# Performance work log

Hardware: AMD Instinct MI355X
Metric: run time of the kernel (lower is better)

## Reference

```python
import jax, jax.numpy as jnp
import numpy as np

B, S, D, H = 8, 2048, 1024, 64


def setup_inputs() -> dict:
    key = jax.random.key(0)
    ks = jax.random.split(key, 9)
    s = 0.02
    return {
        "x": jax.random.normal(ks[0], (B, S, D), jnp.float32),
        "Wq": jax.random.normal(ks[1], (H, D), jnp.float32) * s,
        "bq": jnp.zeros((H,), jnp.float32),
        "Wk": jax.random.normal(ks[2], (H, D), jnp.float32) * s,
        "bk": jnp.zeros((H,), jnp.float32),
        "Wv": jax.random.normal(ks[3], (H, D), jnp.float32) * s,
        "bv": jnp.zeros((H,), jnp.float32),
        "Wo": jax.random.normal(ks[4], (H, H), jnp.float32) * s,
        "bo": jnp.zeros((H,), jnp.float32),
    }


def reference(x, Wq, bq, Wk, bk, Wv, bv, Wo, bo):
    # Linear layers: y = x @ W.T + b (torch nn.Linear convention)
    q = jnp.einsum("bsd,hd->bsh", x, Wq) + bq  # [B,S,H]
    k = jnp.einsum("bsd,hd->bsh", x, Wk) + bk
    v = jnp.einsum("bsd,hd->bsh", x, Wv) + bv
    scale = jnp.float32(H) ** 0.5
    scores = jnp.einsum("bsh,bth->bst", q, k) / scale  # [B,S,S]
    causal = jnp.tril(jnp.ones((S, S), bool))
    scores = jnp.where(causal, scores, -jnp.inf)
    attn = jax.nn.softmax(scores, axis=-1)
    out = jnp.einsum("bst,bth->bsh", attn, v)  # [B,S,H]
    out = jnp.einsum("bsh,gh->bsg", out, Wo) + bo  # output proj [H,H]
    return out
```

## Files before the change

kernel.cpp:

```cpp
#include <hip/hip_runtime.h>
#include <hip/hip_bf16.h>

#define NB 8
#define NS 2048
#define ND 1024
#define NH 64
#define NM (NB*NS)

typedef __attribute__((ext_vector_type(8))) short short8;
typedef __attribute__((ext_vector_type(4))) short short4v;
typedef __attribute__((ext_vector_type(4))) float f32x4;
typedef __attribute__((ext_vector_type(4))) float f4;

#define QSCALE (0.125f * 1.44269504088896340736f)

__device__ __forceinline__ unsigned short f2bf(float f) {
    union { __hip_bfloat16 h; unsigned short u; } cv;
    cv.h = __float2bfloat16(f);
    return cv.u;
}

__global__ __launch_bounds__(256) void convw_kernel(
    const float* __restrict__ Wq, const float* __restrict__ bq,
    const float* __restrict__ Wk, const float* __restrict__ bk,
    const float* __restrict__ Wv, const float* __restrict__ bv,
    const float* __restrict__ Wo,
    unsigned short* __restrict__ Wb, unsigned short* __restrict__ Wob,
    float* __restrict__ biasb)
{
    const int row = blockIdx.x;
    const int t = threadIdx.x;
    if (row < 192) {
        const float* W = row < 64 ? Wq : (row < 128 ? Wk : Wv);
        const float sc = row < 64 ? QSCALE : 1.0f;
        f4 v = *(const f4*)&W[(size_t)(row & 63) * ND + t * 4];
        short4v o;
#pragma unroll
        for (int j = 0; j < 4; ++j) o[j] = (short)f2bf(v[j] * sc);
        *(short4v*)&Wb[(size_t)row * ND + t * 4] = o;
        if (row == 0 && t < 192) {
            const float* bsrc = t < 64 ? bq : (t < 128 ? bk : bv);
            biasb[t] = bsrc[t & 63] * (t < 64 ? QSCALE : 1.0f);
        }
    } else if (t < 16) {
        f4 v = *(const f4*)&Wo[(size_t)(row - 192) * 64 + t * 4];
        short4v o;
#pragma unroll
        for (int j = 0; j < 4; ++j) o[j] = (short)f2bf(v[j]);
        *(short4v*)&Wob[(size_t)(row - 192) * 64 + t * 4] = o;
    }
}

__global__ __launch_bounds__(512, 2) void qkv_kernel(
    const float* __restrict__ x, const unsigned short* __restrict__ Wb,
    const float* __restrict__ biasb,
    unsigned short* __restrict__ q, unsigned short* __restrict__ k,
    unsigned short* __restrict__ vT)
{
    __shared__ unsigned short As[2][64 * 64];
    __shared__ unsigned short Bs[2][192 * 64];

    const int t = threadIdx.x;
    const int lane = t & 63, g = lane >> 4, li = lane & 15;
    const int w = t >> 6, rg = w >> 2, cg = w & 3;
    const int m0 = blockIdx.x * 64;
    const int arow = t >> 3, ach = t & 7;

    f32x4 acc[2][3];
#pragma unroll
    for (int a = 0; a < 2; ++a)
#pragma unroll
        for (int nf = 0; nf < 3; ++nf) acc[a][nf] = (f32x4)0.f;

    f4 xa[2][2]; short8 wr[2][3];

#define QKV_LOAD(KS, SL)                                                          \
    {                                                                             \
        const float* p_ = &x[(size_t)(m0 + arow) * ND + (KS) * 64 + ach * 8];     \
        xa[SL][0] = *(const f4*)p_; xa[SL][1] = *(const f4*)(p_ + 4);             \
        wr[SL][0] = *(const short8*)&Wb[(size_t)(t >> 3) * ND + (KS) * 64 + (t & 7) * 8];                  \
        wr[SL][1] = *(const short8*)&Wb[(size_t)((t + 512) >> 3) * ND + (KS) * 64 + ((t + 512) & 7) * 8];  \
        wr[SL][2] = *(const short8*)&Wb[(size_t)((t + 1024) >> 3) * ND + (KS) * 64 + ((t + 1024) & 7) * 8];\
    }

#define QKV_COMMIT(SL, BUF)                                                       \
    {                                                                             \
        short8 av_;                                                               \
        for (int j_ = 0; j_ < 4; ++j_) {                                          \
            av_[j_] = (short)f2bf(xa[SL][0][j_]);                                 \
            av_[j_ + 4] = (short)f2bf(xa[SL][1][j_]);                             \
        }                                                                         \
        *(short8*)&As[BUF][arow * 64 + ((ach ^ (arow & 7)) << 3)] = av_;          \
        int r0_ = t >> 3, c0_ = t & 7;                                            \
        *(short8*)&Bs[BUF][r0_ * 64 + ((c0_ ^ (r0_ & 7)) << 3)] = wr[SL][0];      \
        int r1_ = (t + 512) >> 3, c1_ = (t + 512) & 7;                            \
        *(short8*)&Bs[BUF][r1_ * 64 + ((c1_ ^ (r1_ & 7)) << 3)] = wr[SL][1];      \
        int r2_ = (t + 1024) >> 3, c2_ = (t + 1024) & 7;                          \
        *(short8*)&Bs[BUF][r2_ * 64 + ((c2_ ^ (r2_ & 7)) << 3)] = wr[SL][2];      \
    }

    QKV_LOAD(0, 0);
    QKV_LOAD(1, 1);
    QKV_COMMIT(0, 0);
    __syncthreads();

#pragma unroll
    for (int ks = 0; ks < 16; ++ks) {
        const int cur = ks & 1;
        if (ks < 14) QKV_LOAD(ks + 2, cur);
#pragma unroll
        for (int h = 0; h < 2; ++h) {
            short8 af0 = *(const short8*)&As[cur][(rg * 32 + 0 + li) * 64 + (((g + 4 * h) ^ (li & 7)) << 3)];
            short8 af1 = *(const short8*)&As[cur][(rg * 32 + 16 + li) * 64 + (((g + 4 * h) ^ (li & 7)) << 3)];
#pragma unroll
            for (int nf = 0; nf < 3; ++nf) {
                short8 bf = *(const short8*)&Bs[cur][(cg * 48 + nf * 16 + li) * 64 + (((g + 4 * h) ^ (li & 7)) << 3)];
                acc[0][nf] = __builtin_amdgcn_mfma_f32_16x16x32_bf16(af0, bf, acc[0][nf], 0, 0, 0);
                acc[1][nf] = __builtin_amdgcn_mfma_f32_16x16x32_bf16(af1, bf, acc[1][nf], 0, 0, 0);
            }
        }
        if (ks < 15) QKV_COMMIT((ks + 1) & 1, cur ^ 1);
        __syncthreads();
    }

#pragma unroll
    for (int nf = 0; nf < 3; ++nf) {
        const int col = cg * 48 + nf * 16 + li;
        const float bias = biasb[col];
#pragma unroll
        for (int a = 0; a < 2; ++a) {
            const int row0 = m0 + rg * 32 + a * 16 + 4 * g;
            if (col < 64) {
#pragma unroll
                for (int i = 0; i < 4; ++i)
                    q[(size_t)(row0 + i) * NH + col] = f2bf(acc[a][nf][i] + bias);
            } else if (col < 128) {
#pragma unroll
                for (int i = 0; i < 4; ++i)
                    k[(size_t)(row0 + i) * NH + (col - 64)] = f2bf(acc[a][nf][i] + bias);
            } else {
                short4v pk;
#pragma unroll
                for (int i = 0; i < 4; ++i) pk[i] = (short)f2bf(acc[a][nf][i] + bias);
                const int bb = row0 >> 11, s = row0 & 2047;
                *(short4v*)&vT[(size_t)(bb * NH + (col - 128)) * NS + s] = pk;
            }
        }
    }
}

__global__ __launch_bounds__(256, 2) void attn_kernel(
    const unsigned short* __restrict__ q, const unsigned short* __restrict__ k,
    const unsigned short* __restrict__ vT,
    float* __restrict__ Opart, float* __restrict__ lpart,
    int ctLog, int MAXC)
{
    __shared__ unsigned short Ks[2][64 * 64];
    __shared__ unsigned short Vs[2][64 * 64];
    __shared__ unsigned short Ps[4][16 * 64];

    const int t = threadIdx.x;
    const int w = t >> 6, lane = t & 63, g = lane >> 4, li = lane & 15;
    const int b = blockIdx.x & 7;
    const int pid = blockIdx.x >> 3;
    const int CT = 1 << ctLog;

    int qt = 0, c = 0;
    {
        int acc = 0;
        for (int u = 31; u >= 0; --u) {
            int nch = (u + CT) >> ctLog;
            if (pid < acc + nch) { qt = u; c = pid - acc; break; }
            acc += nch;
        }
    }
    const int t0 = c * CT;
    const int rem = qt + 1 - t0;
    const int tcount = rem < CT ? rem : CT;

    const size_t qkbase = (size_t)b * NS * NH;
    const int qrow = qt * 64 + w * 16 + li;
    const short8 qa0 = *(const short8*)&q[qkbase + (size_t)qrow * NH + g * 8];
    const short8 qa1 = *(const short8*)&q[qkbase + (size_t)qrow * NH + 32 + g * 8];

    float l_i[4]; f32x4 oacc[4];
#pragma unroll
    for (int i = 0; i < 4; ++i) { l_i[i] = 0.f; oacc[i] = (f32x4)0.f; }

    const int srow = t >> 3, sch = t & 7;
    short8 kreg0, kreg1, vreg0, vreg1;

    {
        const int kv0 = t0 * 64;
        kreg0 = *(const short8*)&k[qkbase + (size_t)(kv0 + srow) * NH + sch * 8];
        kreg1 = *(const short8*)&k[qkbase + (size_t)(kv0 + srow + 32) * NH + sch * 8];
        vreg0 = *(const short8*)&vT[(size_t)(b * NH + srow) * NS + kv0 + sch * 8];
        vreg1 = *(const short8*)&vT[(size_t)(b * NH + srow + 32) * NS + kv0 + sch * 8];
        *(short8*)&Ks[0][srow * 64 + ((sch ^ (srow & 7)) << 3)] = kreg0;
        *(short8*)&Ks[0][(srow + 32) * 64 + ((sch ^ (srow & 7)) << 3)] = kreg1;
        *(short8*)&Vs[0][srow * 64 + ((sch ^ (srow & 7)) << 3)] = vreg0;
        *(short8*)&Vs[0][(srow + 32) * 64 + ((sch ^ (srow & 7)) << 3)] = vreg1;
    }
    __syncthreads();

    for (int tt = 0; tt < tcount; ++tt) {
        const int cur = tt & 1;
        const int kv0 = (t0 + tt) * 64;
        if (tt + 1 < tcount) {
            const int nv0 = kv0 + 64;
            kreg0 = *(const short8*)&k[qkbase + (size_t)(nv0 + srow) * NH + sch * 8];
            kreg1 = *(const short8*)&k[qkbase + (size_t)(nv0 + srow + 32) * NH + sch * 8];
            vreg0 = *(const short8*)&vT[(size_t)(b * NH + srow) * NS + nv0 + sch * 8];
            vreg1 = *(const short8*)&vT[(size_t)(b * NH + srow + 32) * NS + nv0 + sch * 8];
        }
        f32x4 s[4];
#pragma unroll
        for (int c4 = 0; c4 < 4; ++c4) {
            s[c4] = (f32x4)0.f;
            const int krow = 16 * c4 + li;
            short8 kf0 = *(const short8*)&Ks[cur][krow * 64 + ((g ^ (li & 7)) << 3)];
            s[c4] = __builtin_amdgcn_mfma_f32_16x16x32_bf16(qa0, kf0, s[c4], 0, 0, 0);
            short8 kf1 = *(const short8*)&Ks[cur][krow * 64 + (((g + 4) ^ (li & 7)) << 3)];
            s[c4] = __builtin_amdgcn_mfma_f32_16x16x32_bf16(qa1, kf1, s[c4], 0, 0, 0);
        }
        if (kv0 == qt * 64) {
#pragma unroll
            for (int c4 = 0; c4 < 4; ++c4)
#pragma unroll
                for (int i = 0; i < 4; ++i)
                    if (16 * c4 + li > w * 16 + 4 * g + i) s[c4][i] = -1e30f;
        }
        float p[4][4];
#pragma unroll
        for (int c4 = 0; c4 < 4; ++c4)
#pragma unroll
            for (int i = 0; i < 4; ++i)
                p[c4][i] = exp2f(fminf(s[c4][i], 80.f));
#pragma unroll
        for (int i = 0; i < 4; ++i)
            l_i[i] += (p[0][i] + p[1][i]) + (p[2][i] + p[3][i]);

#pragma unroll
        for (int c4 = 0; c4 < 4; ++c4)
#pragma unroll
            for (int i = 0; i < 4; ++i) {
                const int prow = 4 * g + i;
                const int chunk = 2 * c4 + (li >> 3);
                Ps[w][prow * 64 + ((chunk ^ (prow & 7)) << 3) + (li & 7)] = f2bf(p[c4][i]);
            }
        short8 pf0 = *(const short8*)&Ps[w][li * 64 + ((g ^ (li & 7)) << 3)];
        short8 pf1 = *(const short8*)&Ps[w][li * 64 + (((g + 4) ^ (li & 7)) << 3)];
#pragma unroll
        for (int nf = 0; nf < 4; ++nf) {
            const int vrow = nf * 16 + li;
            short8 vf0 = *(const short8*)&Vs[cur][vrow * 64 + ((g ^ (li & 7)) << 3)];
            short8 vf1 = *(const short8*)&Vs[cur][vrow * 64 + (((g + 4) ^ (li & 7)) << 3)];
            oacc[nf] = __builtin_amdgcn_mfma_f32_16x16x32_bf16(pf0, vf0, oacc[nf], 0, 0, 0);
            oacc[nf] = __builtin_amdgcn_mfma_f32_16x16x32_bf16(pf1, vf1, oacc[nf], 0, 0, 0);
        }
        if (tt + 1 < tcount) {
            *(short8*)&Ks[cur ^ 1][srow * 64 + ((sch ^ (srow & 7)) << 3)] = kreg0;
            *(short8*)&Ks[cur ^ 1][(srow + 32) * 64 + ((sch ^ (srow & 7)) << 3)] = kreg1;
            *(short8*)&Vs[cur ^ 1][srow * 64 + ((sch ^ (srow & 7)) << 3)] = vreg0;
            *(short8*)&Vs[cur ^ 1][(srow + 32) * 64 + ((sch ^ (srow & 7)) << 3)] = vreg1;
        }
        __syncthreads();
    }

#pragma unroll
    for (int off = 1; off < 16; off <<= 1)
#pragma unroll
        for (int i = 0; i < 4; ++i) l_i[i] += __shfl_xor(l_i[i], off);

    const size_t slot = (size_t)((b * 32 + qt) * MAXC + c);
    float* Op = Opart + slot * 4096;
#pragma unroll
    for (int nf = 0; nf < 4; ++nf)
#pragma unroll
        for (int i = 0; i < 4; ++i)
            Op[(w * 16 + 4 * g + i) * 64 + nf * 16 + li] = oacc[nf][i];
    if (li == 0) {
#pragma unroll
        for (int i = 0; i < 4; ++i)
            lpart[slot * 64 + w * 16 + 4 * g + i] = l_i[i];
    }
}

__global__ __launch_bounds__(256, 2) void combine_kernel(
    const float* __restrict__ Opart, const float* __restrict__ lpart,
    const unsigned short* __restrict__ Wob, const float* __restrict__ bo,
    float* __restrict__ out, int ctLog, int MAXC)
{
    __shared__ unsigned short Osm[64 * 64];
    __shared__ float Linv[64];

    const int t = threadIdx.x;
    const int b = blockIdx.x & 7, qt = blockIdx.x >> 3;
    const int CT = 1 << ctLog;
    const int nch = (qt + CT) >> ctLog;
    const size_t base_slot = (size_t)(b * 32 + qt) * MAXC;

    if (t < 64) {
        float L = 0.f;
        for (int cc = 0; cc < nch; ++cc)
            L += lpart[(base_slot + cc) * 64 + t];
        Linv[t] = 1.f / L;
    }

    const int r = t >> 2, c0 = (t & 3) * 16;
    f4 a0 = (f4)0.f, a1 = (f4)0.f, a2 = (f4)0.f, a3 = (f4)0.f;
    for (int cc = 0; cc < nch; ++cc) {
        const float* P = Opart + (base_slot + cc) * 4096 + r * 64 + c0;
        a0 += *(const f4*)P; a1 += *(const f4*)(P + 4);
        a2 += *(const f4*)(P + 8); a3 += *(const f4*)(P + 12);
    }
    __syncthreads();
    {
        const float sc = Linv[r];
        short8 o0, o1;
#pragma unroll
        for (int j = 0; j < 4; ++j) {
            o0[j] = (short)f2bf(a0[j] * sc); o0[j + 4] = (short)f2bf(a1[j] * sc);
            o1[j] = (short)f2bf(a2[j] * sc); o1[j + 4] = (short)f2bf(a3[j] * sc);
        }
        const int ch0 = (t & 3) * 2;
        *(short8*)&Osm[r * 64 + ((ch0 ^ (r & 7)) << 3)] = o0;
        *(short8*)&Osm[r * 64 + (((ch0 + 1) ^ (r & 7)) << 3)] = o1;
    }
    __syncthreads();

    const int w = t >> 6, lane = t & 63, g = lane >> 4, li = lane & 15;
    f32x4 acc[4];
#pragma unroll
    for (int nf = 0; nf < 4; ++nf) acc[nf] = (f32x4)0.f;
#pragma unroll
    for (int s = 0; s < 2; ++s) {
        const int rr = w * 16 + li;
        short8 af = *(const short8*)&Osm[rr * 64 + (((g + 4 * s) ^ (rr & 7)) << 3)];
#pragma unroll
        for (int nf = 0; nf < 4; ++nf) {
            short8 bf = *(const short8*)&Wob[(size_t)(nf * 16 + li) * 64 + s * 32 + g * 8];
            acc[nf] = __builtin_amdgcn_mfma_f32_16x16x32_bf16(af, bf, acc[nf], 0, 0, 0);
        }
    }
#pragma unroll
    for (int nf = 0; nf < 4; ++nf) {
        const float bias = bo[nf * 16 + li];
#pragma unroll
        for (int i = 0; i < 4; ++i) {
            const size_t row = (size_t)b * NS + qt * 64 + w * 16 + 4 * g + i;
            out[row * 64 + nf * 16 + li] = acc[nf][i] + bias;
        }
    }
}

extern "C" void kernel_launch(void* const* d_in, const int* in_sizes, int n_in,
                              void* d_out, int out_size, void* d_ws, size_t ws_size,
                              hipStream_t stream)
{
    const float* x  = (const float*)d_in[0];
    const float* Wq = (const float*)d_in[1];
    const float* bq = (const float*)d_in[2];
    const float* Wk = (const float*)d_in[3];
    const float* bk = (const float*)d_in[4];
    const float* Wv = (const float*)d_in[5];
    const float* bv = (const float*)d_in[6];
    const float* Wo = (const float*)d_in[7];
    const float* bo = (const float*)d_in[8];
    float* out = (float*)d_out;

    size_t off = 0;
    auto alloc = [&](size_t bytes) {
        char* p = (char*)d_ws + off;
        off += (bytes + 255) & ~(size_t)255;
        return (void*)p;
    };
    unsigned short* qb  = (unsigned short*)alloc((size_t)NM * NH * 2);
    unsigned short* kb  = (unsigned short*)alloc((size_t)NM * NH * 2);
    unsigned short* vtb = (unsigned short*)alloc((size_t)NM * NH * 2);
    unsigned short* Wb  = (unsigned short*)alloc((size_t)192 * ND * 2);
    unsigned short* Wob = (unsigned short*)alloc((size_t)64 * 64 * 2);
    float* biasb = (float*)alloc(192 * 4);
    const size_t base = off;

    int ctLog = 5, MAXC = 1;
    const int cands[3] = {3, 4, 5};
    for (int ci = 0; ci < 3; ++ci) {
        const int cl = cands[ci];
        const int mc = (31 >> cl) + 1;
        const size_t nslot = (size_t)256 * mc;
        const size_t need = base + nslot * (4096 + 64) * 4 + 8192;
        if (need <= ws_size) { ctLog = cl; MAXC = mc; break; }
    }
    const size_t NSLOT = (size_t)256 * MAXC;
    float* Opart = (float*)alloc(NSLOT * 4096 * 4);
    float* lpart = (float*)alloc(NSLOT * 64 * 4);

    const int CT = 1 << ctLog;
    int NCperB = 0;
    for (int qt = 0; qt < 32; ++qt) NCperB += (qt + CT) >> ctLog;

    convw_kernel<<<256, 256, 0, stream>>>(Wq, bq, Wk, bk, Wv, bv, Wo, Wb, Wob, biasb);
    qkv_kernel<<<NM / 64, 512, 0, stream>>>(x, Wb, biasb, qb, kb, vtb);
    attn_kernel<<<8 * NCperB, 256, 0, stream>>>(qb, kb, vtb, Opart, lpart, ctLog, MAXC);
    combine_kernel<<<256, 256, 0, stream>>>(Opart, lpart, Wob, bo, out, ctLog, MAXC);
}
```

Baseline: 49.24 us.

## Drop LDS staging in QKV projection, load MFMA fragments directly from global

The QKV projection GEMM no longer stages x and weight tiles through double-buffered shared memory with barriers. Each wave now loads its MFMA operand fragments straight from global memory (converting x to bf16 in registers), and blocks shrink to 32 rows and 256 threads. This removes LDS traffic and synchronisation, but each of the four waves re-reads the same x rows, so x is fetched redundantly through cache. The loads also become strided per-lane accesses with no software prefetch.

```diff
diff --git a/kernel.cpp b/kernel.cpp
--- a/kernel.cpp
+++ b/kernel.cpp
@@ -51,20 +51,16 @@
     }
 }
 
-__global__ __launch_bounds__(512, 2) void qkv_kernel(
+__global__ __launch_bounds__(256) void qkv_kernel(
     const float* __restrict__ x, const unsigned short* __restrict__ Wb,
     const float* __restrict__ biasb,
     unsigned short* __restrict__ q, unsigned short* __restrict__ k,
     unsigned short* __restrict__ vT)
 {
-    __shared__ unsigned short As[2][64 * 64];
-    __shared__ unsigned short Bs[2][192 * 64];
-
     const int t = threadIdx.x;
     const int lane = t & 63, g = lane >> 4, li = lane & 15;
-    const int w = t >> 6, rg = w >> 2, cg = w & 3;
-    const int m0 = blockIdx.x * 64;
-    const int arow = t >> 3, ach = t & 7;
+    const int cg = t >> 6;
+    const int m0 = blockIdx.x * 32;
 
     f32x4 acc[2][3];
 #pragma unroll
@@ -72,55 +68,43 @@
 #pragma unroll
         for (int nf = 0; nf < 3; ++nf) acc[a][nf] = (f32x4)0.f;
 
-    f4 xa[2][2]; short8 wr[2][3];
-
-#define QKV_LOAD(KS, SL)                                                          \
-    {                                                                             \
-        const float* p_ = &x[(size_t)(m0 + arow) * ND + (KS) * 64 + ach * 8];     \
-        xa[SL][0] = *(const f4*)p_; xa[SL][1] = *(const f4*)(p_ + 4);             \
-        wr[SL][0] = *(const short8*)&Wb[(size_t)(t >> 3) * ND + (KS) * 64 + (t & 7) * 8];                  \
-        wr[SL][1] = *(const short8*)&Wb[(size_t)((t + 512) >> 3) * ND + (KS) * 64 + ((t + 512) & 7) * 8];  \
-        wr[SL][2] = *(const short8*)&Wb[(size_t)((t + 1024) >> 3) * ND + (KS) * 64 + ((t + 1024) & 7) * 8];\
-    }
-
-#define QKV_COMMIT(SL, BUF)                                                       \
-    {                                                                             \
-        short8 av_;                                                               \
-        for (int j_ = 0; j_ < 4; ++j_) {                                          \
-            av_[j_] = (short)f2bf(xa[SL][0][j_]);                                 \
-            av_[j_ + 4] = (short)f2bf(xa[SL][1][j_]);                             \
-        }                                                                         \
-        *(short8*)&As[BUF][arow * 64 + ((ach ^ (arow & 7)) << 3)] = av_;          \
-        int r0_ = t >> 3, c0_ = t & 7;                                            \
-        *(short8*)&Bs[BUF][r0_ * 64 + ((c0_ ^ (r0_ & 7)) << 3)] = wr[SL][0];      \
-        int r1_ = (t + 512) >> 3, c1_ = (t + 512) & 7;                            \
-        *(short8*)&Bs[BUF][r1_ * 64 + ((c1_ ^ (r1_ & 7)) << 3)] = wr[SL][1];      \
-        int r2_ = (t + 1024) >> 3, c2_ = (t + 1024) & 7;                          \
-        *(short8*)&Bs[BUF][r2_ * 64 + ((c2_ ^ (r2_ & 7)) << 3)] = wr[SL][2];      \
-    }
-
-    QKV_LOAD(0, 0);
-    QKV_LOAD(1, 1);
-    QKV_COMMIT(0, 0);
-    __syncthreads();
+    const float* xr0 = x + (size_t)(m0 + li) * ND;
+    const float* xr1 = x + (size_t)(m0 + 16 + li) * ND;
+    const unsigned short* w0 = Wb + (size_t)(cg * 48 + li) * ND;
+    const unsigned short* w1 = Wb + (size_t)(cg * 48 + 16 + li) * ND;
+    const unsigned short* w2 = Wb + (size_t)(cg * 48 + 32 + li) * ND;
 
 #pragma unroll
     for (int ks = 0; ks < 16; ++ks) {
-        const int cur = ks & 1;
-        if (ks < 14) QKV_LOAD(ks + 2, cur);
+        const int kb = ks * 64;
+        short8 xa[2][2];
+#pragma unroll
+        for (int a = 0; a < 2; ++a)
+#pragma unroll
+            for (int h = 0; h < 2; ++h) {
+                const float* p = (a ? xr1 : xr0) + kb + (g + 4 * h) * 8;
+                f4 v0 = *(const f4*)p, v1 = *(const f4*)(p + 4);
+                short8 av;
+#pragma unroll
+                for (int j = 0; j < 4; ++j) {
+                    av[j]     = (short)f2bf(v0[j]);
+                    av[j + 4] = (short)f2bf(v1[j]);
+                }
+                xa[a][h] = av;
+            }
 #pragma unroll
         for (int h = 0; h < 2; ++h) {
-            short8 af0 = *(const short8*)&As[cur][(rg * 32 + 0 + li) * 64 + (((g + 4 * h) ^ (li & 7)) << 3)];
-            short8 af1 = *(const short8*)&As[cur][(rg * 32 + 16 + li) * 64 + (((g + 4 * h) ^ (li & 7)) << 3)];
-#pragma unroll
-            for (int nf = 0; nf < 3; ++nf) {
-                short8 bf = *(const short8*)&Bs[cur][(cg * 48 + nf * 16 + li) * 64 + (((g + 4 * h) ^ (li & 7)) << 3)];
-                acc[0][nf] = __builtin_amdgcn_mfma_f32_16x16x32_bf16(af0, bf, acc[0][nf], 0, 0, 0);
-                acc[1][nf] = __builtin_amdgcn_mfma_f32_16x16x32_bf16(af1, bf, acc[1][nf], 0, 0, 0);
-            }
-        }
-        if (ks < 15) QKV_COMMIT((ks + 1) & 1, cur ^ 1);
-        __syncthreads();
+            const int off = kb + (g + 4 * h) * 8;
+            short8 b0 = *(const short8*)(w0 + off);
+            short8 b1 = *(const short8*)(w1 + off);
+            short8 b2 = *(const short8*)(w2 + off);
+            acc[0][0] = __builtin_amdgcn_mfma_f32_16x16x32_bf16(xa[0][h], b0, acc[0][0], 0, 0, 0);
+            acc[1][0] = __builtin_amdgcn_mfma_f32_16x16x32_bf16(xa[1][h], b0, acc[1][0], 0, 0, 0);
+            acc[0][1] = __builtin_amdgcn_mfma_f32_16x16x32_bf16(xa[0][h], b1, acc[0][1], 0, 0, 0);
+            acc[1][1] = __builtin_amdgcn_mfma_f32_16x16x32_bf16(xa[1][h], b1, acc[1][1], 0, 0, 0);
+            acc[0][2] = __builtin_amdgcn_mfma_f32_16x16x32_bf16(xa[0][h], b2, acc[0][2], 0, 0, 0);
+            acc[1][2] = __builtin_amdgcn_mfma_f32_16x16x32_bf16(xa[1][h], b2, acc[1][2], 0, 0, 0);
+        }
     }
 
 #pragma unroll
@@ -129,7 +113,7 @@
         const float bias = biasb[col];
 #pragma unroll
         for (int a = 0; a < 2; ++a) {
-            const int row0 = m0 + rg * 32 + a * 16 + 4 * g;
+            const int row0 = m0 + a * 16 + 4 * g;
             if (col < 64) {
 #pragma unroll
                 for (int i = 0; i < 4; ++i)
@@ -401,7 +385,7 @@
     for (int qt = 0; qt < 32; ++qt) NCperB += (qt + CT) >> ctLog;
 
     convw_kernel<<<256, 256, 0, stream>>>(Wq, bq, Wk, bk, Wv, bv, Wo, Wb, Wob, biasb);
-    qkv_kernel<<<NM / 64, 512, 0, stream>>>(x, Wb, biasb, qb, kb, vtb);
+    qkv_kernel<<<NM / 32, 256, 0, stream>>>(x, Wb, biasb, qb, kb, vtb);
     attn_kernel<<<8 * NCperB, 256, 0, stream>>>(qb, kb, vtb, Opart, lpart, ctLog, MAXC);
     combine_kernel<<<256, 256, 0, stream>>>(Opart, lpart, Wob, bo, out, ctLog, MAXC);
 }
```

Result: slower. 86.77 us (+76.2%).

## Halve QKV projection row tile and allow finer attention KV chunking

Applied to the files above, without the earlier changes.

The QKV projection kernel now processes 32 rows per block instead of 64. That doubles the grid to 512 blocks, halves the A tile in shared memory, and raises the launch-bounds occupancy hint to 4 blocks per CU. The aim is to spread the memory-bound fp32 read of x over more CUs and waves. In exchange, each block loads the full 192x64 weight tile per k-step for half as many rows, so weight traffic per output row doubles. The host also adds a chunk size of 4 as a candidate for the attention split, which gives more KV chunks and partial results when the workspace allows it, at the cost of more combine work.

```diff
diff --git a/kernel.cpp b/kernel.cpp
--- a/kernel.cpp
+++ b/kernel.cpp
@@ -51,33 +51,30 @@
     }
 }
 
-__global__ __launch_bounds__(512, 2) void qkv_kernel(
+__global__ __launch_bounds__(512, 4) void qkv_kernel(
     const float* __restrict__ x, const unsigned short* __restrict__ Wb,
     const float* __restrict__ biasb,
     unsigned short* __restrict__ q, unsigned short* __restrict__ k,
     unsigned short* __restrict__ vT)
 {
-    __shared__ unsigned short As[2][64 * 64];
+    __shared__ unsigned short As[2][32 * 64];
     __shared__ unsigned short Bs[2][192 * 64];
 
     const int t = threadIdx.x;
     const int lane = t & 63, g = lane >> 4, li = lane & 15;
     const int w = t >> 6, rg = w >> 2, cg = w & 3;
-    const int m0 = blockIdx.x * 64;
-    const int arow = t >> 3, ach = t & 7;
-
-    f32x4 acc[2][3];
-#pragma unroll
-    for (int a = 0; a < 2; ++a)
-#pragma unroll
-        for (int nf = 0; nf < 3; ++nf) acc[a][nf] = (f32x4)0.f;
-
-    f4 xa[2][2]; short8 wr[2][3];
+    const int m0 = blockIdx.x * 32;
+    const int arow = t >> 4, ac = t & 15;
+
+    f32x4 acc[3];
+#pragma unroll
+    for (int nf = 0; nf < 3; ++nf) acc[nf] = (f32x4)0.f;
+
+    f4 xa[2]; short8 wr[2][3];
 
 #define QKV_LOAD(KS, SL)                                                          \
     {                                                                             \
-        const float* p_ = &x[(size_t)(m0 + arow) * ND + (KS) * 64 + ach * 8];     \
-        xa[SL][0] = *(const f4*)p_; xa[SL][1] = *(const f4*)(p_ + 4);             \
+        xa[SL] = *(const f4*)&x[(size_t)(m0 + arow) * ND + (KS) * 64 + ac * 4];   \
         wr[SL][0] = *(const short8*)&Wb[(size_t)(t >> 3) * ND + (KS) * 64 + (t & 7) * 8];                  \
         wr[SL][1] = *(const short8*)&Wb[(size_t)((t + 512) >> 3) * ND + (KS) * 64 + ((t + 512) & 7) * 8];  \
         wr[SL][2] = *(const short8*)&Wb[(size_t)((t + 1024) >> 3) * ND + (KS) * 64 + ((t + 1024) & 7) * 8];\
@@ -85,12 +82,9 @@
 
 #define QKV_COMMIT(SL, BUF)                                                       \
     {                                                                             \
-        short8 av_;                                                               \
-        for (int j_ = 0; j_ < 4; ++j_) {                                          \
-            av_[j_] = (short)f2bf(xa[SL][0][j_]);                                 \
-            av_[j_ + 4] = (short)f2bf(xa[SL][1][j_]);                             \
-        }                                                                         \
-        *(short8*)&As[BUF][arow * 64 + ((ach ^ (arow & 7)) << 3)] = av_;          \
+        short4v av_;                                                              \
+        for (int j_ = 0; j_ < 4; ++j_) av_[j_] = (short)f2bf(xa[SL][j_]);         \
+        *(short4v*)&As[BUF][arow * 64 + (((ac >> 1) ^ (arow & 7)) << 3) + (ac & 1) * 4] = av_; \
         int r0_ = t >> 3, c0_ = t & 7;                                            \
         *(short8*)&Bs[BUF][r0_ * 64 + ((c0_ ^ (r0_ & 7)) << 3)] = wr[SL][0];      \
         int r1_ = (t + 512) >> 3, c1_ = (t + 512) & 7;                            \
@@ -110,13 +104,11 @@
         if (ks < 14) QKV_LOAD(ks + 2, cur);
 #pragma unroll
         for (int h = 0; h < 2; ++h) {
-            short8 af0 = *(const short8*)&As[cur][(rg * 32 + 0 + li) * 64 + (((g + 4 * h) ^ (li & 7)) << 3)];
-            short8 af1 = *(const short8*)&As[cur][(rg * 32 + 16 + li) * 64 + (((g + 4 * h) ^ (li & 7)) << 3)];
+            short8 af = *(const short8*)&As[cur][(rg * 16 + li) * 64 + (((g + 4 * h) ^ (li & 7)) << 3)];
 #pragma unroll
             for (int nf = 0; nf < 3; ++nf) {
                 short8 bf = *(const short8*)&Bs[cur][(cg * 48 + nf * 16 + li) * 64 + (((g + 4 * h) ^ (li & 7)) << 3)];
-                acc[0][nf] = __builtin_amdgcn_mfma_f32_16x16x32_bf16(af0, bf, acc[0][nf], 0, 0, 0);
-                acc[1][nf] = __builtin_amdgcn_mfma_f32_16x16x32_bf16(af1, bf, acc[1][nf], 0, 0, 0);
+                acc[nf] = __builtin_amdgcn_mfma_f32_16x16x32_bf16(af, bf, acc[nf], 0, 0, 0);
             }
         }
         if (ks < 15) QKV_COMMIT((ks + 1) & 1, cur ^ 1);
@@ -127,24 +119,21 @@
     for (int nf = 0; nf < 3; ++nf) {
         const int col = cg * 48 + nf * 16 + li;
         const float bias = biasb[col];
-#pragma unroll
-        for (int a = 0; a < 2; ++a) {
-            const int row0 = m0 + rg * 32 + a * 16 + 4 * g;
-            if (col < 64) {
-#pragma unroll
-                for (int i = 0; i < 4; ++i)
-                    q[(size_t)(row0 + i) * NH + col] = f2bf(acc[a][nf][i] + bias);
-            } else if (col < 128) {
-#pragma unroll
-                for (int i = 0; i < 4; ++i)
-                    k[(size_t)(row0 + i) * NH + (col - 64)] = f2bf(acc[a][nf][i] + bias);
-            } else {
-                short4v pk;
-#pragma unroll
-                for (int i = 0; i < 4; ++i) pk[i] = (short)f2bf(acc[a][nf][i] + bias);
-                const int bb = row0 >> 11, s = row0 & 2047;
-                *(short4v*)&vT[(size_t)(bb * NH + (col - 128)) * NS + s] = pk;
-            }
+        const int row0 = m0 + rg * 16 + 4 * g;
+        if (col < 64) {
+#pragma unroll
+            for (int i = 0; i < 4; ++i)
+                q[(size_t)(row0 + i) * NH + col] = f2bf(acc[nf][i] + bias);
+        } else if (col < 128) {
+#pragma unroll
+            for (int i = 0; i < 4; ++i)
+                k[(size_t)(row0 + i) * NH + (col - 64)] = f2bf(acc[nf][i] + bias);
+        } else {
+            short4v pk;
+#pragma unroll
+            for (int i = 0; i < 4; ++i) pk[i] = (short)f2bf(acc[nf][i] + bias);
+            const int bb = row0 >> 11, s = row0 & 2047;
+            *(short4v*)&vT[(size_t)(bb * NH + (col - 128)) * NS + s] = pk;
         }
     }
 }
@@ -384,8 +373,8 @@
     const size_t base = off;
 
     int ctLog = 5, MAXC = 1;
-    const int cands[3] = {3, 4, 5};
-    for (int ci = 0; ci < 3; ++ci) {
+    const int cands[4] = {2, 3, 4, 5};
+    for (int ci = 0; ci < 4; ++ci) {
         const int cl = cands[ci];
         const int mc = (31 >> cl) + 1;
         const size_t nslot = (size_t)256 * mc;
@@ -401,7 +390,7 @@
     for (int qt = 0; qt < 32; ++qt) NCperB += (qt + CT) >> ctLog;
 
     convw_kernel<<<256, 256, 0, stream>>>(Wq, bq, Wk, bk, Wv, bv, Wo, Wb, Wob, biasb);
-    qkv_kernel<<<NM / 64, 512, 0, stream>>>(x, Wb, biasb, qb, kb, vtb);
+    qkv_kernel<<<NM / 32, 512, 0, stream>>>(x, Wb, biasb, qb, kb, vtb);
     attn_kernel<<<8 * NCperB, 256, 0, stream>>>(qb, kb, vtb, Opart, lpart, ctLog, MAXC);
     combine_kernel<<<256, 256, 0, stream>>>(Opart, lpart, Wob, bo, out, ctLog, MAXC);
 }
```

New measurement: 52.22 us. 1.06x slower.
